# Kernel tuning notes

Hardware: AMD Instinct MI355X
Metric: run time of the kernel (lower is better)

## Reference

```python
import jax, jax.numpy as jnp
import numpy as np

B, K, D = 512, 16, 256
E = 32            # num_experts
H = int(D * 0.25) # d_hidden = 64


def setup_inputs() -> dict:
    key = jax.random.key(0)
    ks = jax.random.split(key, 7)
    d_rs = D ** -0.5
    h_rs = H ** -0.5
    x = jax.random.normal(ks[0], (B, K, D), dtype=jnp.float32)
    router_w = jax.random.uniform(ks[1], (E, D), jnp.float32, -d_rs, d_rs)
    router_b = jax.random.uniform(ks[2], (E,), jnp.float32, -d_rs, d_rs)
    # init_rsqrt_uniform_(weights1, weights1.shape[-1]) -> bound = H**-0.5
    W1 = jax.random.uniform(ks[3], (E, D, H), jnp.float32, -h_rs, h_rs)
    b1 = jax.random.uniform(ks[4], (E, H), jnp.float32, -h_rs, h_rs)
    # init_rsqrt_uniform_(weights2, weights2.shape[-1]) -> bound = D**-0.5
    W2 = jax.random.uniform(ks[5], (E, H, D), jnp.float32, -d_rs, d_rs)
    b2 = jax.random.uniform(ks[6], (E, D), jnp.float32, -d_rs, d_rs)
    return {"x": x, "router_w": router_w, "router_b": router_b,
            "W1": W1, "b1": b1, "W2": W2, "b2": b2}


def reference(x, router_w, router_b, W1, b1, W2, b2):
    # x: [B, K, D] -> flatten tokens: [N, D]
    xf = x.reshape(-1, D)
    logits = xf @ router_w.T + router_b          # [N, E]
    idx = jnp.argmax(logits, axis=-1)            # [N] top-1 expert per token
    # Gather per-token expert weights (honors top-1 sparsity: N*D*H FLOPs,
    # not E*N*D*H dense dispatch).
    w1t = jnp.take(W1, idx, axis=0)              # [N, D, H]
    h = jnp.einsum('nd,ndh->nh', xf, w1t) + jnp.take(b1, idx, axis=0)
    h = jax.nn.relu(h)                           # act1; dropout p=0 is identity
    w2t = jnp.take(W2, idx, axis=0)              # [N, H, D]
    out = jnp.einsum('nh,nhd->nd', h, w2t) + jnp.take(b2, idx, axis=0)
    out = jax.nn.relu(out)                       # original applies act1 again
    return out.reshape(x.shape)
```

## Files before the change

### kernel.cpp

```cpp
#include <hip/hip_runtime.h>
#include <hip/hip_bf16.h>


constexpr int D = 256;
constexpr int H = 64;
constexpr int E = 32;
constexpr int T_TILE = 16;
constexpr int MAX_TILES = 544;
constexpr int HIST = 0;
constexpr int EIDX = 8192;
constexpr int PERM = 16384;
constexpr int WCNT = 24576;

__device__ __forceinline__ float quad_reduce(float v) {
    int i1 = __builtin_bit_cast(int, v);
    v += __builtin_bit_cast(float,
        __builtin_amdgcn_mov_dpp(i1, 0xB1, 0xF, 0xF, true));
    int i2 = __builtin_bit_cast(int, v);
    v += __builtin_bit_cast(float,
        __builtin_amdgcn_mov_dpp(i2, 0x4E, 0xF, 0xF, true));
    return v;
}

__global__ __launch_bounds__(256) void router_kernel(
    const float* __restrict__ x, const float* __restrict__ rw,
    const float* __restrict__ rb, int* __restrict__ ws)
{
    __shared__ float4 xs[32][65];
    __shared__ float4 rwt[64][33];
    __shared__ float logitS[32][E + 1];
    __shared__ int lcnt[E];

    const int t = threadIdx.x;
    const int n0 = blockIdx.x * 32;
    if (t < E) lcnt[t] = 0;

    const float4* x4 = (const float4*)x;
    const float4* rw4 = (const float4*)rw;
    for (int i = t; i < 32 * 64; i += 256) {
        int r = i >> 6, q = i & 63;
        xs[r][q] = x4[(size_t)(n0 + r) * 64 + q];
        rwt[q][r] = rw4[i];
    }
    __syncthreads();

    {
        const int e = t & 31, g = t >> 5;
        float s[4];
#pragma unroll
        for (int j = 0; j < 4; ++j) s[j] = rb[e];
#pragma unroll
        for (int p = 0; p < 8; ++p) {
            float sp[4] = {0.f, 0.f, 0.f, 0.f};
#pragma unroll
            for (int k4 = 0; k4 < 8; ++k4) {
                float4 wv = rwt[p * 8 + k4][e];
#pragma unroll
                for (int j = 0; j < 4; ++j) {
                    float4 xv = xs[g * 4 + j][p * 8 + k4];
                    sp[j] = fmaf(xv.x, wv.x, sp[j]);
                    sp[j] = fmaf(xv.y, wv.y, sp[j]);
                    sp[j] = fmaf(xv.z, wv.z, sp[j]);
                    sp[j] = fmaf(xv.w, wv.w, sp[j]);
                }
            }
#pragma unroll
            for (int j = 0; j < 4; ++j) s[j] += sp[j];
        }
#pragma unroll
        for (int j = 0; j < 4; ++j) logitS[g * 4 + j][e] = s[j];
    }
    __syncthreads();

    if (t < 32) {
        float best = logitS[t][0];
        int bi = 0;
#pragma unroll
        for (int i = 1; i < E; ++i) {
            float v = logitS[t][i];
            if (v > best) { best = v; bi = i; }
        }
        ws[EIDX + n0 + t] = bi;
        atomicAdd(&lcnt[bi], 1);
    }
    __syncthreads();
    if (t < E) ws[HIST + blockIdx.x * E + t] = lcnt[t];
}

__global__ __launch_bounds__(256) void scatter_kernel(int* __restrict__ ws)
{
    __shared__ int cfull[8][E], cbelow[8][E];
    __shared__ int cnts_s[E], below_s[E], offs_s[E], lcnt[E];

    const int t = threadIdx.x;
    const int b = blockIdx.x;
    const int c = t >> 5, e = t & 31;
    const int rlim = 8 * b;

    int full = 0, below = 0;
    for (int i = 0; i < 32; ++i) {
        const int r = c * 32 + i;
        const int v = ws[HIST + r * E + e];
        full += v;
        if (r < rlim) below += v;
    }
    cfull[c][e] = full; cbelow[c][e] = below;
    __syncthreads();
    if (t < E) {
        int tot = 0, bg = 0;
#pragma unroll
        for (int c2 = 0; c2 < 8; ++c2) { tot += cfull[c2][t]; bg += cbelow[c2][t]; }
        cnts_s[t] = tot; below_s[t] = bg; lcnt[t] = 0;
    }
    __syncthreads();
    if (t == 0) {
        int off = 0;
        for (int e2 = 0; e2 < E; ++e2) { offs_s[e2] = off; off += cnts_s[e2]; }
    }
    __syncthreads();
    {
        const int n = b * 256 + t;
        const int e2 = ws[EIDX + n];
        const int r = atomicAdd(&lcnt[e2], 1);
        ws[PERM + offs_s[e2] + below_s[e2] + r] = n;
    }
    if (b == 0 && t < E) ws[WCNT + t] = cnts_s[t];
}

__global__ __launch_bounds__(256) void ffn_kernel(
    const float* __restrict__ x,
    const float* __restrict__ W1, const float* __restrict__ b1,
    const float* __restrict__ W2, const float* __restrict__ b2,
    const int* __restrict__ ws, float* __restrict__ out)
{
    __shared__ float part[4][T_TILE][H];
    __shared__ float hsl[T_TILE][H];
    __shared__ int rowsl[T_TILE];
    __shared__ int cs[E];

    const int t = threadIdx.x;
    if (t < E) cs[t] = ws[WCNT + t];
    __syncthreads();

    int e = -1, start = 0, cnt = 0;
    {
        int b = blockIdx.x, off = 0;
#pragma unroll 1
        for (int e2 = 0; e2 < E; ++e2) {
            const int c = cs[e2];
            const int nt = (c + T_TILE - 1) >> 4;
            if (e < 0) {
                if (b < nt) { e = e2; start = off + b * T_TILE;
                              cnt = min(T_TILE, c - b * T_TILE); }
                else b -= nt;
            }
            off += c;
        }
    }
    if (e < 0) return;

    const int lane = t & 63;
    const int w = t >> 6;
    const int s = lane & 3;
    const int q = lane >> 2;

    if (t < T_TILE)
        rowsl[t] = ws[PERM + start + (t < cnt ? t : 0)];

    const float* w1e = W1 + (size_t)e * (D * H);
    float4 w1v[16];
    {
        const float* base = w1e + (size_t)((w * 4 + s) * 16) * H + 4 * q;
#pragma unroll
        for (int k = 0; k < 16; ++k)
            w1v[k] = *(const float4*)(base + k * H);
    }
    __syncthreads();

#define LOADX(buf, row) {                                                  \
        const float* xb_ = x + (size_t)(row) * D + (w * 4 + s) * 16;       \
        buf[0] = *(const float4*)(xb_ + 0);                                \
        buf[1] = *(const float4*)(xb_ + 4);                                \
        buf[2] = *(const float4*)(xb_ + 8);                                \
        buf[3] = *(const float4*)(xb_ + 12); }

#define BODY1(tok, xb) {                                                   \
        float sp0 = 0.f, sp1 = 0.f, sp2 = 0.f, sp3 = 0.f;                  \
        _Pragma("unroll")                                                  \
        for (int k4 = 0; k4 < 4; ++k4) {                                   \
            float4 xv = xb[k4];                                            \
            _Pragma("unroll")                                              \
            for (int m = 0; m < 4; ++m) {                                  \
                const int k = k4 * 4 + m;                                  \
                const float xs_ = (m == 0) ? xv.x : (m == 1) ? xv.y        \
                                 : (m == 2) ? xv.z : xv.w;                 \
                sp0 = fmaf(xs_, w1v[k].x, sp0);                            \
                sp1 = fmaf(xs_, w1v[k].y, sp1);                            \
                sp2 = fmaf(xs_, w1v[k].z, sp2);                            \
                sp3 = fmaf(xs_, w1v[k].w, sp3);                            \
            }                                                              \
        }                                                                  \
        sp0 = quad_reduce(sp0); sp1 = quad_reduce(sp1);                    \
        sp2 = quad_reduce(sp2); sp3 = quad_reduce(sp3);                    \
        float a_ = (s & 1) ? sp1 : sp0;                                    \
        float c_ = (s & 1) ? sp3 : sp2;                                    \
        part[w][tok][4 * q + s] = (s & 2) ? c_ : a_; }

    {
        float4 xa[4], xb4[4];
        LOADX(xa, rowsl[0]);
        for (int tok = 0; tok < cnt; tok += 2) {
            if (tok + 1 < cnt) LOADX(xb4, rowsl[tok + 1]);
            BODY1(tok, xa);
            if (tok + 1 < cnt) {
                if (tok + 2 < cnt) LOADX(xa, rowsl[tok + 2]);
                BODY1(tok + 1, xb4);
            }
        }
    }

    const float* w2e = W2 + (size_t)e * (H * D);
    float4 w2v[16];
    {
        const float* base = w2e + (size_t)(16 * s) * D + 64 * w + 4 * q;
#pragma unroll
        for (int k = 0; k < 16; ++k)
            w2v[k] = *(const float4*)(base + k * D);
    }
    const float b2v = b2[e * D + 64 * w + 4 * q + s];
    __syncthreads();

    {
        const int h = t & 63;
        const int tq = t >> 6;
        const float b1v = b1[e * H + h];
#pragma unroll
        for (int r = 0; r < 4; ++r) {
            const int tok = tq * 4 + r;
            if (tok < cnt) {
                float v = part[0][tok][h] + part[1][tok][h]
                        + part[2][tok][h] + part[3][tok][h] + b1v;
                hsl[tok][h] = fmaxf(v, 0.f);
            }
        }
    }
    __syncthreads();

#define LOADH(buf, tok) {                                                  \
        const float* hb_ = &hsl[tok][s * 16];                              \
        buf[0] = *(const float4*)(hb_ + 0);                                \
        buf[1] = *(const float4*)(hb_ + 4);                                \
        buf[2] = *(const float4*)(hb_ + 8);                                \
        buf[3] = *(const float4*)(hb_ + 12); }

#define BODY2(tok, hb) {                                                   \
        float sp0 = 0.f, sp1 = 0.f, sp2 = 0.f, sp3 = 0.f;                  \
        _Pragma("unroll")                                                  \
        for (int k4 = 0; k4 < 4; ++k4) {                                   \
            float4 hv = hb[k4];                                            \
            _Pragma("unroll")                                              \
            for (int m = 0; m < 4; ++m) {                                  \
                const int k = k4 * 4 + m;                                  \
                const float hs_ = (m == 0) ? hv.x : (m == 1) ? hv.y        \
                                 : (m == 2) ? hv.z : hv.w;                 \
                sp0 = fmaf(hs_, w2v[k].x, sp0);                            \
                sp1 = fmaf(hs_, w2v[k].y, sp1);                            \
                sp2 = fmaf(hs_, w2v[k].z, sp2);                            \
                sp3 = fmaf(hs_, w2v[k].w, sp3);                            \
            }                                                              \
        }                                                                  \
        sp0 = quad_reduce(sp0); sp1 = quad_reduce(sp1);                    \
        sp2 = quad_reduce(sp2); sp3 = quad_reduce(sp3);                    \
        float a_ = (s & 1) ? sp1 : sp0;                                    \
        float c_ = (s & 1) ? sp3 : sp2;                                    \
        const float val_ = ((s & 2) ? c_ : a_) + b2v;                      \
        const int row_ = rowsl[tok];                                       \
        out[(size_t)row_ * D + 64 * w + 4 * q + s] = fmaxf(val_, 0.f); }

    {
        float4 ha[4], hb4[4];
        LOADH(ha, 0);
        for (int tok = 0; tok < cnt; tok += 2) {
            if (tok + 1 < cnt) LOADH(hb4, tok + 1);
            BODY2(tok, ha);
            if (tok + 1 < cnt) {
                if (tok + 2 < cnt) LOADH(ha, tok + 2);
                BODY2(tok + 1, hb4);
            }
        }
    }
#undef LOADX
#undef BODY1
#undef LOADH
#undef BODY2
}

extern "C" void kernel_launch(void* const* d_in, const int* in_sizes, int n_in,
                              void* d_out, int out_size, void* d_ws, size_t ws_size,
                              hipStream_t stream) {
    const float* x  = (const float*)d_in[0];
    const float* rw = (const float*)d_in[1];
    const float* rb = (const float*)d_in[2];
    const float* W1 = (const float*)d_in[3];
    const float* b1 = (const float*)d_in[4];
    const float* W2 = (const float*)d_in[5];
    const float* b2 = (const float*)d_in[6];
    float* out = (float*)d_out;
    int* ws = (int*)d_ws;

    const int N = in_sizes[0] / D;

    router_kernel<<<N / 32, 256, 0, stream>>>(x, rw, rb, ws);
    scatter_kernel<<<N / 256, 256, 0, stream>>>(ws);
    ffn_kernel<<<MAX_TILES, 256, 0, stream>>>(x, W1, b1, W2, b2, ws, out);
}
```

Measured before the change: 111.6 us.

## Fuse router, scatter and expert FFN into one persistent kernel with grid barrier

```diff
diff --git a/kernel.cpp b/kernel.cpp
--- a/kernel.cpp
+++ b/kernel.cpp
@@ -6,11 +6,11 @@
 constexpr int H = 64;
 constexpr int E = 32;
 constexpr int T_TILE = 16;
-constexpr int MAX_TILES = 544;
+constexpr int NBLK = 256;
 constexpr int HIST = 0;
 constexpr int EIDX = 8192;
-constexpr int PERM = 16384;
-constexpr int WCNT = 24576;
+constexpr int ARR  = 16384;
+constexpr int MAGIC = 0x51C0FFEE;
 
 __device__ __forceinline__ float quad_reduce(float v) {
     int i1 = __builtin_bit_cast(int, v);
@@ -22,160 +22,186 @@
     return v;
 }
 
-__global__ __launch_bounds__(256) void router_kernel(
-    const float* __restrict__ x, const float* __restrict__ rw,
-    const float* __restrict__ rb, int* __restrict__ ws)
+union SU {
+    struct {
+        float4 xs[32][65];
+        float4 rwt[64][33];
+        float  logitS[32][E + 1];
+    } r;
+    struct {
+        float part[4][T_TILE][H];
+        float hsl[T_TILE][H];
+    } f;
+};
+
+__global__ __launch_bounds__(256) void fused_moe(
+    const float* __restrict__ x,  const float* __restrict__ rw,
+    const float* __restrict__ rb, const float* __restrict__ W1,
+    const float* __restrict__ b1, const float* __restrict__ W2,
+    const float* __restrict__ b2, int* __restrict__ wsp,
+    float* __restrict__ out)
 {
-    __shared__ float4 xs[32][65];
-    __shared__ float4 rwt[64][33];
-    __shared__ float logitS[32][E + 1];
+    __shared__ SU su;
     __shared__ int lcnt[E];
+    __shared__ int cfull[8][E];
+    __shared__ int cs[E];
+    __shared__ int scan_s[256];
+    __shared__ int rowsl[T_TILE];
+    __shared__ int ntile_s;
 
     const int t = threadIdx.x;
-    const int n0 = blockIdx.x * 32;
-    if (t < E) lcnt[t] = 0;
-
-    const float4* x4 = (const float4*)x;
-    const float4* rw4 = (const float4*)rw;
-    for (int i = t; i < 32 * 64; i += 256) {
-        int r = i >> 6, q = i & 63;
-        xs[r][q] = x4[(size_t)(n0 + r) * 64 + q];
-        rwt[q][r] = rw4[i];
-    }
-    __syncthreads();
+    const int g = blockIdx.x;
+    const int n0 = g * 32;
 
     {
-        const int e = t & 31, g = t >> 5;
-        float s[4];
-#pragma unroll
-        for (int j = 0; j < 4; ++j) s[j] = rb[e];
-#pragma unroll
-        for (int p = 0; p < 8; ++p) {
-            float sp[4] = {0.f, 0.f, 0.f, 0.f};
-#pragma unroll
-            for (int k4 = 0; k4 < 8; ++k4) {
-                float4 wv = rwt[p * 8 + k4][e];
-#pragma unroll
-                for (int j = 0; j < 4; ++j) {
-                    float4 xv = xs[g * 4 + j][p * 8 + k4];
-                    sp[j] = fmaf(xv.x, wv.x, sp[j]);
-                    sp[j] = fmaf(xv.y, wv.y, sp[j]);
-                    sp[j] = fmaf(xv.z, wv.z, sp[j]);
-                    sp[j] = fmaf(xv.w, wv.w, sp[j]);
-                }
-            }
-#pragma unroll
-            for (int j = 0; j < 4; ++j) s[j] += sp[j];
-        }
-#pragma unroll
-        for (int j = 0; j < 4; ++j) logitS[g * 4 + j][e] = s[j];
-    }
-    __syncthreads();
-
-    if (t < 32) {
-        float best = logitS[t][0];
-        int bi = 0;
-#pragma unroll
-        for (int i = 1; i < E; ++i) {
-            float v = logitS[t][i];
-            if (v > best) { best = v; bi = i; }
-        }
-        ws[EIDX + n0 + t] = bi;
-        atomicAdd(&lcnt[bi], 1);
-    }
-    __syncthreads();
-    if (t < E) ws[HIST + blockIdx.x * E + t] = lcnt[t];
-}
-
-__global__ __launch_bounds__(256) void scatter_kernel(int* __restrict__ ws)
-{
-    __shared__ int cfull[8][E], cbelow[8][E];
-    __shared__ int cnts_s[E], below_s[E], offs_s[E], lcnt[E];
-
-    const int t = threadIdx.x;
-    const int b = blockIdx.x;
-    const int c = t >> 5, e = t & 31;
-    const int rlim = 8 * b;
-
-    int full = 0, below = 0;
-    for (int i = 0; i < 32; ++i) {
-        const int r = c * 32 + i;
-        const int v = ws[HIST + r * E + e];
-        full += v;
-        if (r < rlim) below += v;
-    }
-    cfull[c][e] = full; cbelow[c][e] = below;
+        if (t < E) lcnt[t] = 0;
+        const float4* x4 = (const float4*)x;
+        const float4* rw4 = (const float4*)rw;
+        for (int i = t; i < 32 * 64; i += 256) {
+            int r = i >> 6, qq = i & 63;
+            su.r.xs[r][qq] = x4[(size_t)(n0 + r) * 64 + qq];
+            su.r.rwt[qq][r] = rw4[i];
+        }
+        __syncthreads();
+
+        {
+            const int e = t & 31, gg = t >> 5;
+            float s[4];
+#pragma unroll
+            for (int j = 0; j < 4; ++j) s[j] = rb[e];
+#pragma unroll
+            for (int p = 0; p < 8; ++p) {
+                float sp[4] = {0.f, 0.f, 0.f, 0.f};
+#pragma unroll
+                for (int k4 = 0; k4 < 8; ++k4) {
+                    float4 wv = su.r.rwt[p * 8 + k4][e];
+#pragma unroll
+                    for (int j = 0; j < 4; ++j) {
+                        float4 xv = su.r.xs[gg * 4 + j][p * 8 + k4];
+                        sp[j] = fmaf(xv.x, wv.x, sp[j]);
+                        sp[j] = fmaf(xv.y, wv.y, sp[j]);
+                        sp[j] = fmaf(xv.z, wv.z, sp[j]);
+                        sp[j] = fmaf(xv.w, wv.w, sp[j]);
+                    }
+                }
+#pragma unroll
+                for (int j = 0; j < 4; ++j) s[j] += sp[j];
+            }
+#pragma unroll
+            for (int j = 0; j < 4; ++j) su.r.logitS[gg * 4 + j][e] = s[j];
+        }
+        __syncthreads();
+
+        if (t < 32) {
+            float best = su.r.logitS[t][0];
+            int bi = 0;
+#pragma unroll
+            for (int i = 1; i < E; ++i) {
+                float v = su.r.logitS[t][i];
+                if (v > best) { best = v; bi = i; }
+            }
+            wsp[EIDX + n0 + t] = bi;
+            atomicAdd(&lcnt[bi], 1);
+        }
+        __syncthreads();
+        if (t < E) wsp[HIST + g * E + t] = lcnt[t];
+    }
+
+    __syncthreads();
+    __threadfence();
+    if (t == 0)
+        __hip_atomic_store(&wsp[ARR + g], MAGIC,
+                           __ATOMIC_RELEASE, __HIP_MEMORY_SCOPE_AGENT);
+    while (__hip_atomic_load(&wsp[ARR + t],
+                             __ATOMIC_ACQUIRE, __HIP_MEMORY_SCOPE_AGENT)
+           != MAGIC)
+        __builtin_amdgcn_s_sleep(2);
+    __syncthreads();
+
+    {
+        const int c = t >> 5, e2 = t & 31;
+        int full = 0;
+        for (int i = 0; i < 32; ++i)
+            full += wsp[HIST + (c * 32 + i) * E + e2];
+        cfull[c][e2] = full;
+    }
     __syncthreads();
     if (t < E) {
-        int tot = 0, bg = 0;
-#pragma unroll
-        for (int c2 = 0; c2 < 8; ++c2) { tot += cfull[c2][t]; bg += cbelow[c2][t]; }
-        cnts_s[t] = tot; below_s[t] = bg; lcnt[t] = 0;
+        int tot = 0;
+#pragma unroll
+        for (int c2 = 0; c2 < 8; ++c2) tot += cfull[c2][t];
+        cs[t] = tot;
     }
     __syncthreads();
     if (t == 0) {
-        int off = 0;
-        for (int e2 = 0; e2 < E; ++e2) { offs_s[e2] = off; off += cnts_s[e2]; }
-    }
-    __syncthreads();
-    {
-        const int n = b * 256 + t;
-        const int e2 = ws[EIDX + n];
-        const int r = atomicAdd(&lcnt[e2], 1);
-        ws[PERM + offs_s[e2] + below_s[e2] + r] = n;
-    }
-    if (b == 0 && t < E) ws[WCNT + t] = cnts_s[t];
-}
-
-__global__ __launch_bounds__(256) void ffn_kernel(
-    const float* __restrict__ x,
-    const float* __restrict__ W1, const float* __restrict__ b1,
-    const float* __restrict__ W2, const float* __restrict__ b2,
-    const int* __restrict__ ws, float* __restrict__ out)
-{
-    __shared__ float part[4][T_TILE][H];
-    __shared__ float hsl[T_TILE][H];
-    __shared__ int rowsl[T_TILE];
-    __shared__ int cs[E];
-
-    const int t = threadIdx.x;
-    if (t < E) cs[t] = ws[WCNT + t];
-    __syncthreads();
-
-    int e = -1, start = 0, cnt = 0;
-    {
-        int b = blockIdx.x, off = 0;
-#pragma unroll 1
-        for (int e2 = 0; e2 < E; ++e2) {
-            const int c = cs[e2];
-            const int nt = (c + T_TILE - 1) >> 4;
-            if (e < 0) {
-                if (b < nt) { e = e2; start = off + b * T_TILE;
-                              cnt = min(T_TILE, c - b * T_TILE); }
-                else b -= nt;
-            }
-            off += c;
-        }
-    }
-    if (e < 0) return;
+        int nt = 0;
+        for (int e2 = 0; e2 < E; ++e2) nt += (cs[e2] + 15) >> 4;
+        ntile_s = nt;
+    }
+    __syncthreads();
+    const int numTiles = ntile_s;
 
     const int lane = t & 63;
     const int w = t >> 6;
     const int s = lane & 3;
     const int q = lane >> 2;
 
-    if (t < T_TILE)
-        rowsl[t] = ws[PERM + start + (t < cnt ? t : 0)];
-
-    const float* w1e = W1 + (size_t)e * (D * H);
-    float4 w1v[16];
-    {
-        const float* base = w1e + (size_t)((w * 4 + s) * 16) * H + 4 * q;
-#pragma unroll
-        for (int k = 0; k < 16; ++k)
-            w1v[k] = *(const float4*)(base + k * H);
-    }
-    __syncthreads();
+    for (int pass = 0; pass < 3; ++pass) {
+        const int tile = g + pass * NBLK;
+        if (tile >= numTiles) break;
+        __syncthreads();
+
+        int e = -1, slot = 0;
+        {
+            int b = tile;
+#pragma unroll 1
+            for (int e2 = 0; e2 < E; ++e2) {
+                const int nt = (cs[e2] + 15) >> 4;
+                if (e < 0) {
+                    if (b < nt) { e = e2; slot = b; }
+                    else b -= nt;
+                }
+            }
+        }
+        const int lo = slot * 16;
+        const int cnt = min(T_TILE, cs[e] - lo);
+
+        int mycount = 0;
+        {
+            const int* ep = wsp + EIDX + 32 * t;
+#pragma unroll
+            for (int i = 0; i < 32; ++i) mycount += (ep[i] == e);
+        }
+        scan_s[t] = mycount;
+        __syncthreads();
+        for (int d2 = 1; d2 < 256; d2 <<= 1) {
+            int v = scan_s[t];
+            int u = (t >= d2) ? scan_s[t - d2] : 0;
+            __syncthreads();
+            scan_s[t] = v + u;
+            __syncthreads();
+        }
+        {
+            int r = scan_s[t] - mycount;
+            const int* ep = wsp + EIDX + 32 * t;
+#pragma unroll
+            for (int i = 0; i < 32; ++i) {
+                if (ep[i] == e) {
+                    if (r >= lo && r < lo + T_TILE) rowsl[r - lo] = 32 * t + i;
+                    ++r;
+                }
+            }
+        }
+        __syncthreads();
+
+        const float* w1e = W1 + (size_t)e * (D * H);
+        float4 w1v[16];
+        {
+            const float* base = w1e + (size_t)((w * 4 + s) * 16) * H + 4 * q;
+#pragma unroll
+            for (int k = 0; k < 16; ++k)
+                w1v[k] = *(const float4*)(base + k * H);
+        }
 
 #define LOADX(buf, row) {                                                  \
         const float* xb_ = x + (size_t)(row) * D + (w * 4 + s) * 16;       \
@@ -204,50 +230,50 @@
         sp2 = quad_reduce(sp2); sp3 = quad_reduce(sp3);                    \
         float a_ = (s & 1) ? sp1 : sp0;                                    \
         float c_ = (s & 1) ? sp3 : sp2;                                    \
-        part[w][tok][4 * q + s] = (s & 2) ? c_ : a_; }
-
-    {
-        float4 xa[4], xb4[4];
-        LOADX(xa, rowsl[0]);
-        for (int tok = 0; tok < cnt; tok += 2) {
-            if (tok + 1 < cnt) LOADX(xb4, rowsl[tok + 1]);
-            BODY1(tok, xa);
-            if (tok + 1 < cnt) {
-                if (tok + 2 < cnt) LOADX(xa, rowsl[tok + 2]);
-                BODY1(tok + 1, xb4);
-            }
-        }
-    }
-
-    const float* w2e = W2 + (size_t)e * (H * D);
-    float4 w2v[16];
-    {
-        const float* base = w2e + (size_t)(16 * s) * D + 64 * w + 4 * q;
-#pragma unroll
-        for (int k = 0; k < 16; ++k)
-            w2v[k] = *(const float4*)(base + k * D);
-    }
-    const float b2v = b2[e * D + 64 * w + 4 * q + s];
-    __syncthreads();
-
-    {
-        const int h = t & 63;
-        const int tq = t >> 6;
-        const float b1v = b1[e * H + h];
-#pragma unroll
-        for (int r = 0; r < 4; ++r) {
-            const int tok = tq * 4 + r;
-            if (tok < cnt) {
-                float v = part[0][tok][h] + part[1][tok][h]
-                        + part[2][tok][h] + part[3][tok][h] + b1v;
-                hsl[tok][h] = fmaxf(v, 0.f);
-            }
-        }
-    }
-    __syncthreads();
+        su.f.part[w][tok][4 * q + s] = (s & 2) ? c_ : a_; }
+
+        {
+            float4 xa[4], xb4[4];
+            LOADX(xa, rowsl[0]);
+            for (int tok = 0; tok < cnt; tok += 2) {
+                if (tok + 1 < cnt) LOADX(xb4, rowsl[tok + 1]);
+                BODY1(tok, xa);
+                if (tok + 1 < cnt) {
+                    if (tok + 2 < cnt) LOADX(xa, rowsl[tok + 2]);
+                    BODY1(tok + 1, xb4);
+                }
+            }
+        }
+
+        const float* w2e = W2 + (size_t)e * (H * D);
+        float4 w2v[16];
+        {
+            const float* base = w2e + (size_t)(16 * s) * D + 64 * w + 4 * q;
+#pragma unroll
+            for (int k = 0; k < 16; ++k)
+                w2v[k] = *(const float4*)(base + k * D);
+        }
+        const float b2v = b2[e * D + 64 * w + 4 * q + s];
+        __syncthreads();
+
+        {
+            const int h = t & 63;
+            const int tq = t >> 6;
+            const float b1v = b1[e * H + h];
+#pragma unroll
+            for (int r2 = 0; r2 < 4; ++r2) {
+                const int tok = tq * 4 + r2;
+                if (tok < cnt) {
+                    float v = su.f.part[0][tok][h] + su.f.part[1][tok][h]
+                            + su.f.part[2][tok][h] + su.f.part[3][tok][h] + b1v;
+                    su.f.hsl[tok][h] = fmaxf(v, 0.f);
+                }
+            }
+        }
+        __syncthreads();
 
 #define LOADH(buf, tok) {                                                  \
-        const float* hb_ = &hsl[tok][s * 16];                              \
+        const float* hb_ = &su.f.hsl[tok][s * 16];                         \
         buf[0] = *(const float4*)(hb_ + 0);                                \
         buf[1] = *(const float4*)(hb_ + 4);                                \
         buf[2] = *(const float4*)(hb_ + 8);                                \
@@ -277,22 +303,23 @@
         const int row_ = rowsl[tok];                                       \
         out[(size_t)row_ * D + 64 * w + 4 * q + s] = fmaxf(val_, 0.f); }
 
-    {
-        float4 ha[4], hb4[4];
-        LOADH(ha, 0);
-        for (int tok = 0; tok < cnt; tok += 2) {
-            if (tok + 1 < cnt) LOADH(hb4, tok + 1);
-            BODY2(tok, ha);
-            if (tok + 1 < cnt) {
-                if (tok + 2 < cnt) LOADH(ha, tok + 2);
-                BODY2(tok + 1, hb4);
-            }
-        }
-    }
+        {
+            float4 ha[4], hb4[4];
+            LOADH(ha, 0);
+            for (int tok = 0; tok < cnt; tok += 2) {
+                if (tok + 1 < cnt) LOADH(hb4, tok + 1);
+                BODY2(tok, ha);
+                if (tok + 1 < cnt) {
+                    if (tok + 2 < cnt) LOADH(ha, tok + 2);
+                    BODY2(tok + 1, hb4);
+                }
+            }
+        }
 #undef LOADX
 #undef BODY1
 #undef LOADH
 #undef BODY2
+    }
 }
 
 extern "C" void kernel_launch(void* const* d_in, const int* in_sizes, int n_in,
@@ -308,9 +335,5 @@
     float* out = (float*)d_out;
     int* ws = (int*)d_ws;
 
-    const int N = in_sizes[0] / D;
-
-    router_kernel<<<N / 32, 256, 0, stream>>>(x, rw, rb, ws);
-    scatter_kernel<<<N / 256, 256, 0, stream>>>(ws);
-    ffn_kernel<<<MAX_TILES, 256, 0, stream>>>(x, W1, b1, W2, b2, ws, out);
+    fused_moe<<<NBLK, 256, 0, stream>>>(x, rw, rb, W1, b1, W2, b2, ws, out);
 }
```

Measured after the change: 179.7 us. 1.61x slower.
